# Kernel tuning notes

Measured on AMD Instinct MI355X. Metric: run time of the kernel, lower is better.

## Reference

```python
import jax, jax.numpy as jnp
import numpy as np
from jax import lax

N = 100000   # number of points / rows of X and inv[i]
C = 16       # input channels
F = 16       # filters
W = 8        # beam window width
D = 3        # dims (number of pre/post conv pairs)
NSEG = 8192  # number of beam segments (fixed stand-in for reduce_max(I)+1)


def _conv2d_relu(x, w, b):
    # x: [H, W, Cin], w: [kh, kw, Cin, Cout], 'same' padding + relu (keras Conv2D)
    y = lax.conv_general_dilated(x[None], w, (1, 1), 'SAME',
                                 dimension_numbers=('NHWC', 'HWIO', 'NHWC'))[0]
    return jax.nn.relu(y + b)


def setup_inputs() -> dict:
    key = jax.random.key(0)
    ks = jax.random.split(key, 5)
    X = jax.random.normal(ks[0], (N, C), jnp.float32)
    inv = jax.random.randint(ks[1], (D, N, W), 0, N, jnp.int32)
    index = jax.random.randint(ks[2], (D, N), 0, NSEG, jnp.int32)
    pre_w = jax.random.normal(ks[3], (D, 3, 3, C, F), jnp.float32) * 0.05
    pre_b = jnp.zeros((D, F), jnp.float32)
    post_w = jax.random.normal(ks[4], (D, 3, 1, F, F), jnp.float32) * 0.05
    post_b = jnp.zeros((D, F), jnp.float32)
    return {"X": X, "inv": inv, "index": index,
            "pre_w": pre_w, "pre_b": pre_b, "post_w": post_w, "post_b": post_b}


def reference(X, inv, index, pre_w, pre_b, post_w, post_b):
    Y = jnp.zeros((N, W, F), jnp.float32)
    for i in range(D):  # small fixed structural loop over dims
        x = X[inv[i]]                                      # gather_nd -> [N, W, C]
        x = _conv2d_relu(x, pre_w[i], pre_b[i])            # [N, W, F]
        I = index[i]                                       # [N] segment ids
        x = jax.ops.segment_sum(x, I, num_segments=NSEG)   # [NSEG, W, F]
        x = _conv2d_relu(x, post_w[i], post_b[i])          # (3,1) kernel, same pad
        Y = Y + x[I]                                       # gather back -> [N, W, F]
    return Y
```

## Files before the change

kernel.cpp:

```cpp
#include <hip/hip_runtime.h>

#define N_    100000
#define C_    16
#define F_    16
#define W_    8
#define D_    3
#define NSEG_ 8192
#define BR    16

#define SEGROW (W_*F_)
#define SEGBUF ((size_t)NSEG_ * SEGROW)

typedef __attribute__((ext_vector_type(4))) float f32x4;
typedef __attribute__((ext_vector_type(8))) short bf16x8;

static __device__ __forceinline__ short f2bf(float x) {
    union { float f; unsigned u; } v; v.f = x;
    unsigned r = v.u + 0x7fffu + ((v.u >> 16) & 1u);
    return (short)(r >> 16);
}

__global__ __launch_bounds__(256) void preconv_seg_mfma(
    const float* __restrict__ X, const int* __restrict__ inv,
    const int* __restrict__ index, const float* __restrict__ pre_w,
    const float* __restrict__ pre_b, float* __restrict__ seg)
{
    const int i  = blockIdx.y;
    const int r0 = blockIdx.x * BR;
    const int t  = threadIdx.x;

    __shared__ __align__(16) short xg[20][10][16];
    __shared__ __align__(16) short wbT[16][160];
    __shared__ float bs[F_];
    __shared__ int   sidx[BR];

    int* xz = (int*)&xg[0][0][0];
    for (int k = t; k < 20 * 10 * 16 / 2; k += 256) xz[k] = 0;

    for (int k = t; k < 16 * 160; k += 256) {
        const int f = k / 160, kk = k - f * 160;
        wbT[f][kk] = (kk < 144) ? f2bf(pre_w[i * 2304 + kk * 16 + f])
                                : (short)0;
    }
    if (t < F_) bs[t] = pre_b[i * F_ + t];
    if (t < BR) sidx[t] = index[(size_t)i * N_ + r0 + t];
    __syncthreads();

    for (int k = t; k < 288; k += 256) {
        const int pair = k >> 1, half = k & 1;
        const int row = pair >> 3, w = pair & 7;
        const int n = r0 - 1 + row;
        if (n >= 0 && n < N_) {
            const int src = inv[((size_t)i * N_ + n) * W_ + w];
            const float4 v0 = *(const float4*)&X[(size_t)src * C_ + half * 8];
            const float4 v1 = *(const float4*)&X[(size_t)src * C_ + half * 8 + 4];
            bf16x8 o;
            o[0] = f2bf(v0.x); o[1] = f2bf(v0.y); o[2] = f2bf(v0.z); o[3] = f2bf(v0.w);
            o[4] = f2bf(v1.x); o[5] = f2bf(v1.y); o[6] = f2bf(v1.z); o[7] = f2bf(v1.w);
            *(bf16x8*)&xg[row][w + 1][half * 8] = o;
        }
    }
    __syncthreads();

    const int lane = t & 63;
    const int wv   = t >> 6;
    const int fc   = lane & 15;
    const int kb   = lane >> 4;
    const int mA   = lane & 15;
    const int rowC0 = kb * 4;

#pragma unroll
    for (int tt = 0; tt < 2; ++tt) {
        const int m_base = (wv * 2 + tt) * 16;
        const int m  = m_base + mA;
        const int nl = m >> 3;
        const int w  = m & 7;
        f32x4 acc = {0.f, 0.f, 0.f, 0.f};
#pragma unroll
        for (int s = 0; s < 5; ++s) {
            const int g  = s * 4 + kb;
            const int gg = g >> 1;
            const int c0 = (g & 1) * 8;
            const int dr = gg / 3;
            const int dw = gg - dr * 3;
            const bf16x8 a = *(const bf16x8*)&xg[nl + dr][w + dw][c0];
            const bf16x8 b = *(const bf16x8*)&wbT[fc][s * 32 + kb * 8];
            acc = __builtin_amdgcn_mfma_f32_16x16x32_bf16(a, b, acc, 0, 0, 0);
        }
#pragma unroll
        for (int r = 0; r < 4; ++r) {
            const int mc  = m_base + rowC0 + r;
            const int nlc = mc >> 3, wc = mc & 7;
            const float v = fmaxf(acc[r] + bs[fc], 0.f);
            atomicAdd(&seg[((size_t)i * NSEG_ + sidx[nlc]) * SEGROW + wc * F_ + fc], v);
        }
    }
}

__global__ __launch_bounds__(256) void postconv(
    const float* __restrict__ seg, const float* __restrict__ post_w,
    const float* __restrict__ post_b, float* __restrict__ post)
{
    const int i = blockIdx.y;
    const int t = threadIdx.x;

    __shared__ float ws[3][F_][F_];
    __shared__ float bs[F_];
    for (int k = t; k < 3 * F_ * F_; k += 256)
        (&ws[0][0][0])[k] = post_w[i * 3 * F_ * F_ + k];
    if (t < F_) bs[t] = post_b[i * F_ + t];
    __syncthreads();

    const int idx = blockIdx.x * 256 + t;
    const int fo  = idx & 15;
    const int w   = (idx >> 4) & 7;
    const int s   = idx >> 7;

    float acc = bs[fo];
#pragma unroll
    for (int dh = 0; dh < 3; ++dh) {
        const int ss = s + dh - 1;
        if (ss < 0 || ss >= NSEG_) continue;
        const float* sp = seg + ((size_t)i * NSEG_ + ss) * SEGROW + w * F_;
        const float4 s0 = *(const float4*)(sp);
        const float4 s1 = *(const float4*)(sp + 4);
        const float4 s2 = *(const float4*)(sp + 8);
        const float4 s3 = *(const float4*)(sp + 12);
        const float sv[16] = {s0.x, s0.y, s0.z, s0.w, s1.x, s1.y, s1.z, s1.w,
                              s2.x, s2.y, s2.z, s2.w, s3.x, s3.y, s3.z, s3.w};
#pragma unroll
        for (int fi = 0; fi < F_; ++fi)
            acc += sv[fi] * ws[dh][fi][fo];
    }
    post[(size_t)i * SEGBUF + idx] = fmaxf(acc, 0.f);
}

__global__ __launch_bounds__(256) void gather_sum(
    const float* __restrict__ post, const int* __restrict__ index,
    float* __restrict__ Y)
{
    const int gt = blockIdx.x * 256 + threadIdx.x;
    if (gt >= N_ * 32) return;
    const int q = gt & 31;
    const int n = gt >> 5;

    float4 acc = make_float4(0.f, 0.f, 0.f, 0.f);
#pragma unroll
    for (int i = 0; i < D_; ++i) {
        const int s = index[(size_t)i * N_ + n];
        const float4 v = *(const float4*)&post[(size_t)i * SEGBUF +
                                               (size_t)s * SEGROW + q * 4];
        acc.x += v.x; acc.y += v.y; acc.z += v.z; acc.w += v.w;
    }
    *(float4*)&Y[(size_t)n * SEGROW + q * 4] = acc;
}

extern "C" void kernel_launch(void* const* d_in, const int* in_sizes, int n_in,
                              void* d_out, int out_size, void* d_ws, size_t ws_size,
                              hipStream_t stream)
{
    const float* X      = (const float*)d_in[0];
    const int*   inv    = (const int*)  d_in[1];
    const int*   index  = (const int*)  d_in[2];
    const float* pre_w  = (const float*)d_in[3];
    const float* pre_b  = (const float*)d_in[4];
    const float* post_w = (const float*)d_in[5];
    const float* post_b = (const float*)d_in[6];
    float*       Y      = (float*)d_out;

    float* seg  = (float*)d_ws;
    float* post = seg + D_ * SEGBUF;

    hipMemsetAsync(seg, 0, D_ * SEGBUF * sizeof(float), stream);

    preconv_seg_mfma<<<dim3(N_ / BR, D_), 256, 0, stream>>>(
        X, inv, index, pre_w, pre_b, seg);
    postconv<<<dim3((NSEG_ * W_ * F_) / 256, D_), 256, 0, stream>>>(
        seg, post_w, post_b, post);
    gather_sum<<<dim3((N_ * 32 + 255) / 256), 256, 0, stream>>>(post, index, Y);
}
```

Baseline: 291.5 us.

## Replace atomic segment-sum with counting-sort and per-segment gather reduction

Builds a per-dim histogram, prefix scan and scatter to get a segment-sorted order of rows. The pre-conv writes bf16 outputs to a staging buffer, and a separate kernel sums each segment's rows in order into the segment buffer, so the float atomics into seg go away. The cost is more kernel launches (per-dim preconv and segsum, plus sort kernels), an extra bf16 round trip through global memory, and load imbalance across segments of different sizes. Dropping the seg memset also changes determinism and accumulation precision, since the inputs are rounded to bf16 before summing.

```diff
diff --git a/kernel.cpp b/kernel.cpp
--- a/kernel.cpp
+++ b/kernel.cpp
@@ -20,30 +20,76 @@
     return (short)(r >> 16);
 }
 
-__global__ __launch_bounds__(256) void preconv_seg_mfma(
+__global__ __launch_bounds__(256) void hist_k(
+    const int* __restrict__ index, int* __restrict__ hist)
+{
+    const int i = blockIdx.y;
+    const int n = blockIdx.x * 256 + threadIdx.x;
+    if (n < N_) atomicAdd(&hist[i * NSEG_ + index[(size_t)i * N_ + n]], 1);
+}
+
+__global__ __launch_bounds__(256) void scan_k(
+    const int* __restrict__ hist, int* __restrict__ basep)
+{
+    const int i = blockIdx.x;
+    const int t = threadIdx.x;
+    __shared__ int sums[256];
+
+    int run = 0;
+#pragma unroll
+    for (int j = 0; j < 32; ++j) run += hist[i * NSEG_ + t * 32 + j];
+    sums[t] = run;
+    __syncthreads();
+    for (int off = 1; off < 256; off <<= 1) {
+        int v = (t >= off) ? sums[t - off] : 0;
+        __syncthreads();
+        sums[t] += v;
+        __syncthreads();
+    }
+    int acc = sums[t] - run;
+#pragma unroll
+    for (int j = 0; j < 32; ++j) {
+        const int idx = i * NSEG_ + t * 32 + j;
+        const int v = hist[idx];
+        basep[idx] = acc;
+        acc += v;
+    }
+}
+
+__global__ __launch_bounds__(256) void scatter_k(
+    const int* __restrict__ index, const int* __restrict__ basep,
+    int* __restrict__ cursor, int* __restrict__ order)
+{
+    const int i = blockIdx.y;
+    const int n = blockIdx.x * 256 + threadIdx.x;
+    if (n < N_) {
+        const int s = index[(size_t)i * N_ + n];
+        const int off = atomicAdd(&cursor[i * NSEG_ + s], 1);
+        order[(size_t)i * N_ + basep[i * NSEG_ + s] + off] = n;
+    }
+}
+
+__global__ __launch_bounds__(256) void preconv_mfma(
     const float* __restrict__ X, const int* __restrict__ inv,
-    const int* __restrict__ index, const float* __restrict__ pre_w,
-    const float* __restrict__ pre_b, float* __restrict__ seg)
-{
-    const int i  = blockIdx.y;
+    const float* __restrict__ pre_w, const float* __restrict__ pre_b,
+    short* __restrict__ convout)
+{
     const int r0 = blockIdx.x * BR;
     const int t  = threadIdx.x;
 
     __shared__ __align__(16) short xg[20][10][16];
     __shared__ __align__(16) short wbT[16][160];
+    __shared__ __align__(16) short cbuf[128 * 16];
     __shared__ float bs[F_];
-    __shared__ int   sidx[BR];
 
     int* xz = (int*)&xg[0][0][0];
     for (int k = t; k < 20 * 10 * 16 / 2; k += 256) xz[k] = 0;
 
     for (int k = t; k < 16 * 160; k += 256) {
         const int f = k / 160, kk = k - f * 160;
-        wbT[f][kk] = (kk < 144) ? f2bf(pre_w[i * 2304 + kk * 16 + f])
-                                : (short)0;
-    }
-    if (t < F_) bs[t] = pre_b[i * F_ + t];
-    if (t < BR) sidx[t] = index[(size_t)i * N_ + r0 + t];
+        wbT[f][kk] = (kk < 144) ? f2bf(pre_w[kk * 16 + f]) : (short)0;
+    }
+    if (t < F_) bs[t] = pre_b[t];
     __syncthreads();
 
     for (int k = t; k < 288; k += 256) {
@@ -51,7 +97,7 @@
         const int row = pair >> 3, w = pair & 7;
         const int n = r0 - 1 + row;
         if (n >= 0 && n < N_) {
-            const int src = inv[((size_t)i * N_ + n) * W_ + w];
+            const int src = inv[(size_t)n * W_ + w];
             const float4 v0 = *(const float4*)&X[(size_t)src * C_ + half * 8];
             const float4 v1 = *(const float4*)&X[(size_t)src * C_ + half * 8 + 4];
             bf16x8 o;
@@ -67,7 +113,6 @@
     const int fc   = lane & 15;
     const int kb   = lane >> 4;
     const int mA   = lane & 15;
-    const int rowC0 = kb * 4;
 
 #pragma unroll
     for (int tt = 0; tt < 2; ++tt) {
@@ -89,12 +134,38 @@
         }
 #pragma unroll
         for (int r = 0; r < 4; ++r) {
-            const int mc  = m_base + rowC0 + r;
-            const int nlc = mc >> 3, wc = mc & 7;
-            const float v = fmaxf(acc[r] + bs[fc], 0.f);
-            atomicAdd(&seg[((size_t)i * NSEG_ + sidx[nlc]) * SEGROW + wc * F_ + fc], v);
+            const int mc = m_base + kb * 4 + r;
+            cbuf[mc * 16 + fc] = f2bf(fmaxf(acc[r] + bs[fc], 0.f));
         }
     }
+    __syncthreads();
+    *(bf16x8*)&convout[(size_t)r0 * SEGROW + t * 8] = *(bf16x8*)&cbuf[t * 8];
+}
+
+__global__ __launch_bounds__(256) void segsum_k(
+    const short* __restrict__ convout, const int* __restrict__ order,
+    const int* __restrict__ hist, const int* __restrict__ basep,
+    float* __restrict__ seg)
+{
+    const int t = threadIdx.x;
+    const int s = blockIdx.x * 4 + (t >> 6);
+    const int l = t & 63;
+
+    const int cnt  = hist[s];
+    const int base = basep[s];
+    const unsigned* cp = (const unsigned*)convout;
+
+    float a0 = 0.f, a1 = 0.f;
+    for (int p = 0; p < cnt; ++p) {
+        const int n = order[base + p];
+        const unsigned v = cp[(size_t)n * 64 + l];
+        union { unsigned u; float f; } lo, hi;
+        lo.u = v << 16;
+        hi.u = v & 0xffff0000u;
+        a0 += lo.f;
+        a1 += hi.f;
+    }
+    *(float2*)&seg[(size_t)s * SEGROW + 2 * l] = make_float2(a0, a1);
 }
 
 __global__ __launch_bounds__(256) void postconv(
@@ -168,13 +239,31 @@
     const float* post_b = (const float*)d_in[6];
     float*       Y      = (float*)d_out;
 
-    float* seg  = (float*)d_ws;
-    float* post = seg + D_ * SEGBUF;
-
-    hipMemsetAsync(seg, 0, D_ * SEGBUF * sizeof(float), stream);
-
-    preconv_seg_mfma<<<dim3(N_ / BR, D_), 256, 0, stream>>>(
-        X, inv, index, pre_w, pre_b, seg);
+    char* p = (char*)d_ws;
+    float* seg     = (float*)p;               p += D_ * SEGBUF * sizeof(float);
+    float* post    = (float*)p;               p += D_ * SEGBUF * sizeof(float);
+    short* convout = (short*)p;               p += (size_t)N_ * SEGROW * sizeof(short);
+    int*   order   = (int*)p;                 p += (size_t)D_ * N_ * sizeof(int);
+    int*   hist    = (int*)p;                 p += D_ * NSEG_ * sizeof(int);
+    int*   cursor  = (int*)p;                 p += D_ * NSEG_ * sizeof(int);
+    int*   basep   = (int*)p;                 p += D_ * NSEG_ * sizeof(int);
+
+    hipMemsetAsync(hist, 0, 2 * D_ * NSEG_ * sizeof(int), stream);
+
+    const int nb = (N_ + 255) / 256;
+    hist_k   <<<dim3(nb, D_), 256, 0, stream>>>(index, hist);
+    scan_k   <<<D_, 256, 0, stream>>>(hist, basep);
+    scatter_k<<<dim3(nb, D_), 256, 0, stream>>>(index, basep, cursor, order);
+
+    for (int i = 0; i < D_; ++i) {
+        preconv_mfma<<<N_ / BR, 256, 0, stream>>>(
+            X, inv + (size_t)i * N_ * W_, pre_w + i * 2304, pre_b + i * F_,
+            convout);
+        segsum_k<<<NSEG_ / 4, 256, 0, stream>>>(
+            convout, order + (size_t)i * N_, hist + i * NSEG_,
+            basep + i * NSEG_, seg + (size_t)i * SEGBUF);
+    }
+
     postconv<<<dim3((NSEG_ * W_ * F_) / 256, D_), 256, 0, stream>>>(
         seg, post_w, post_b, post);
     gather_sum<<<dim3((N_ * 32 + 255) / 256), 256, 0, stream>>>(post, index, Y);
```

Result: slower. 352.9 us (+21.0%).
